# Performance work log

Measured on AMD Instinct MI355X. Metric: run time of the kernel, lower is better.

The kernel has to match this reference:

```python
import jax, jax.numpy as jnp
import numpy as np

B, T, C, H = 4, 2048, 1024, 16
D = C // H

def setup_inputs() -> dict:
    key = jax.random.key(0)
    k1, k2, k3, k4 = jax.random.split(key, 4)
    s = 1.0 / np.sqrt(C)
    return {
        "x": jax.random.normal(k1, (B, T, C), dtype=jnp.float32),
        "W_qkv": jax.random.normal(k2, (3 * C, C), dtype=jnp.float32) * s,
        "W_out": jax.random.normal(k3, (C, C), dtype=jnp.float32) * s,
        "b_out": jax.random.normal(k4, (C,), dtype=jnp.float32) * s,
    }

def reference(x, W_qkv, W_out, b_out):
    Bx, Tx, Cx = x.shape
    # qkv projection (torch Linear: y = x @ W.T), bias=False
    qkv = x @ W_qkv.T                               # [B,T,3C]
    q, k, v = jnp.split(qkv, 3, axis=-1)
    def heads(t):
        return t.reshape(Bx, Tx, H, D).transpose(0, 2, 1, 3)  # [B,H,T,D]
    q, k, v = heads(q), heads(k), heads(v)
    scale = 1.0 / jnp.sqrt(jnp.asarray(D, dtype=x.dtype))
    scores = jnp.einsum("bhqd,bhkd->bhqk", q, k) * scale      # [B,H,T,T]
    causal = jnp.tril(jnp.ones((Tx, Tx), dtype=bool))
    scores = jnp.where(causal[None, None], scores, -jnp.inf)
    attn = jax.nn.softmax(scores, axis=-1)                    # dropout p=0 (eval)
    out = jnp.einsum("bhqk,bhkd->bhqd", attn, v)              # [B,H,T,D]
    out = out.transpose(0, 2, 1, 3).reshape(Bx, Tx, Cx)       # [B,T,C]
    return out @ W_out.T + b_out
```

## Files before the change

kernel.cpp:

```cpp
#include <hip/hip_runtime.h>


typedef __attribute__((ext_vector_type(8))) __bf16 bf16x8;
typedef __attribute__((ext_vector_type(4))) float f32x4;
typedef __attribute__((ext_vector_type(16))) float f32x16;

__device__ __forceinline__ unsigned short f2bf(float f) {
  union { float f; unsigned u; } v; v.f = f;
  unsigned r = v.u + 0x7fffu + ((v.u >> 16) & 1u);
  return (unsigned short)(r >> 16);
}

__device__ __forceinline__ unsigned cvtpk(float lo, float hi) {
  unsigned r;
  asm("v_cvt_pk_bf16_f32 %0, %1, %2" : "=v"(r) : "v"(lo), "v"(hi));
  return r;
}

__device__ __forceinline__ float fexp2(float x) {
  float r;
  asm("v_exp_f32 %0, %1" : "=v"(r) : "v"(x));
  return r;
}
__device__ __forceinline__ float max3f(float a, float b, float c) {
  return fmaxf(fmaxf(a, b), c);
}

__device__ __forceinline__ void gld16(const void* g, void* l) {
  __builtin_amdgcn_global_load_lds(
      (const __attribute__((address_space(1))) void*)g,
      (__attribute__((address_space(3))) void*)l, 16, 0, 0);
}

__device__ __forceinline__ f32x4 mfma16(bf16x8 a, bf16x8 b, f32x4 c) {
  return __builtin_amdgcn_mfma_f32_16x16x32_bf16(a, b, c, 0, 0, 0);
}
__device__ __forceinline__ f32x16 mfma32(bf16x8 a, bf16x8 b, f32x16 c) {
  return __builtin_amdgcn_mfma_f32_32x32x16_bf16(a, b, c, 0, 0, 0);
}

__global__ __launch_bounds__(256) void cast_f32_bf16(
    const float* __restrict__ src, unsigned short* __restrict__ dst, int n) {
  int i = (blockIdx.x * 256 + threadIdx.x) * 4;
  if (i >= n) return;
  float4 v = *(const float4*)(src + i);
  ushort4 o;
  o.x = f2bf(v.x); o.y = f2bf(v.y); o.z = f2bf(v.z); o.w = f2bf(v.w);
  *(ushort4*)(dst + i) = o;
}

__device__ __forceinline__ bf16x8 ldsw128(const char* mat, int row, int cb) {
  return *(const bf16x8*)(mat + row * 128 + (cb ^ ((row & 7) << 4)));
}
__device__ __forceinline__ int swz512(int r) {
  return ((r & 7) << 4) ^ (((r >> 3) & 3) << 7);
}

#define PH_SYNC_A() do { __builtin_amdgcn_s_barrier();              \
    asm volatile("s_waitcnt lgkmcnt(0)" ::: "memory");              \
    __builtin_amdgcn_sched_barrier(0); } while (0)
#define PH_SYNC_B() do { __builtin_amdgcn_s_barrier();              \
    __builtin_amdgcn_sched_barrier(0); } while (0)
#define VMC6() asm volatile("s_waitcnt vmcnt(6)" ::: "memory")
#define VMC0() asm volatile("s_waitcnt vmcnt(0)" ::: "memory")

#define QUAD(MH, NH, AF, BF) do {                                   \
    __builtin_amdgcn_s_setprio(1);                                  \
    _Pragma("unroll") for (int mt = 0; mt < 4; ++mt)                \
    _Pragma("unroll") for (int nt = 0; nt < 2; ++nt)                \
    _Pragma("unroll") for (int kk = 0; kk < 2; ++kk)                \
      acc[(MH)*4+mt][(NH)*2+nt] =                                   \
          mfma16(AF[mt][kk], BF[nt][kk], acc[(MH)*4+mt][(NH)*2+nt]);\
    __builtin_amdgcn_s_setprio(0);                                  \
  } while (0)

__device__ __forceinline__ void stage_half(const char* gbase, char* mat,
                                           int kt, int half, int tid) {
#pragma unroll
  for (int q = 0; q < 2; ++q) {
    const int r = half * 128 + q * 64 + (tid >> 3);
    const int cb = (tid & 7) * 16;
    gld16(gbase + (size_t)r * 2048 + kt * 128 + (cb ^ ((r & 7) << 4)),
          mat + r * 128 + cb);
  }
}

__device__ __forceinline__ void rdA(bf16x8 aF[4][2], const char* mat,
                                    int wm, int mh, int lr, int lg) {
#pragma unroll
  for (int mt = 0; mt < 4; ++mt) {
    const int row = mh * 128 + wm * 64 + mt * 16 + lr;
#pragma unroll
    for (int kk = 0; kk < 2; ++kk)
      aF[mt][kk] = ldsw128(mat, row, kk * 64 + lg * 16);
  }
}
__device__ __forceinline__ void rdB(bf16x8 bF[2][2], const char* mat,
                                    int wn, int nh, int lr, int lg) {
#pragma unroll
  for (int nt = 0; nt < 2; ++nt) {
    const int row = wn * 64 + nh * 32 + nt * 16 + lr;
#pragma unroll
    for (int kk = 0; kk < 2; ++kk)
      bF[nt][kk] = ldsw128(mat, row, kk * 64 + lg * 16);
  }
}

template <int MODE>
__global__ __launch_bounds__(512, 2) void gemm8p(
    const unsigned short* __restrict__ A, const unsigned short* __restrict__ Bm,
    unsigned short* __restrict__ qo, unsigned short* __restrict__ ko,
    unsigned short* __restrict__ vo,
    const float* __restrict__ bias, float* __restrict__ fout) {
  __shared__ char lds[131072];
  const int tid = threadIdx.x;
  const int w = tid >> 6, l = tid & 63, lr = l & 15, lg = l >> 4;
  const int wm = w >> 2, wn = w & 3;
  constexpr int GX = (MODE == 0) ? 12 : 4;
  const int L = blockIdx.x + blockIdx.y * GX;
  const int x = L & 7, i8 = L >> 3;
  const int m0 = (x * 4 + (i8 & 3)) * 256;
  const int n0 = (i8 >> 2) * 256;
  const char* Ag = (const char*)A + (size_t)m0 * 2048;
  const char* Bg = (const char*)Bm + (size_t)n0 * 2048;
  char* A0 = lds;           char* B0 = lds + 32768;
  char* A1 = lds + 65536;   char* B1 = lds + 98304;

  f32x4 acc[8][4];
  f32x4 zero = {0.f, 0.f, 0.f, 0.f};
#pragma unroll
  for (int i = 0; i < 8; i++)
#pragma unroll
    for (int jj = 0; jj < 4; jj++) acc[i][jj] = zero;

  stage_half(Ag, A0, 0, 0, tid);
  stage_half(Ag, A0, 0, 1, tid);
  stage_half(Bg, B0, 0, 0, tid);
  stage_half(Bg, B0, 0, 1, tid);
  stage_half(Ag, A1, 1, 0, tid);
  stage_half(Bg, B1, 1, 0, tid);
  stage_half(Bg, B1, 1, 1, tid);
  VMC6();
  __builtin_amdgcn_s_barrier();
  __builtin_amdgcn_sched_barrier(0);

  for (int j = 0; j < 8; ++j) {
    const int t0 = 2 * j, t1 = 2 * j + 1;
    const bool more = (j < 7);
    bf16x8 aF[4][2], b0F[2][2], b1F[2][2];

    rdA(aF, A0, wm, 0, lr, lg);
    rdB(b0F, B0, wn, 0, lr, lg);
    stage_half(Ag, A1, t1, 1, tid);
    PH_SYNC_A();
    QUAD(0, 0, aF, b0F);
    PH_SYNC_B();
    rdB(b1F, B0, wn, 1, lr, lg);
    if (more) stage_half(Ag, A0, t0 + 2, 0, tid);
    PH_SYNC_A();
    QUAD(0, 1, aF, b1F);
    PH_SYNC_B();
    rdA(aF, A0, wm, 1, lr, lg);
    if (more) stage_half(Bg, B0, t0 + 2, 0, tid);
    PH_SYNC_A();
    QUAD(1, 1, aF, b1F);
    PH_SYNC_B();
    if (more) stage_half(Bg, B0, t0 + 2, 1, tid);
    PH_SYNC_A();
    QUAD(1, 0, aF, b0F);
    if (more) VMC6(); else VMC0();
    PH_SYNC_B();
    rdA(aF, A1, wm, 0, lr, lg);
    rdB(b0F, B1, wn, 0, lr, lg);
    if (more) stage_half(Ag, A0, t0 + 2, 1, tid);
    PH_SYNC_A();
    QUAD(0, 0, aF, b0F);
    PH_SYNC_B();
    rdB(b1F, B1, wn, 1, lr, lg);
    if (more) stage_half(Ag, A1, t1 + 2, 0, tid);
    PH_SYNC_A();
    QUAD(0, 1, aF, b1F);
    PH_SYNC_B();
    rdA(aF, A1, wm, 1, lr, lg);
    if (more) stage_half(Bg, B1, t1 + 2, 0, tid);
    PH_SYNC_A();
    QUAD(1, 1, aF, b1F);
    PH_SYNC_B();
    if (more) stage_half(Bg, B1, t1 + 2, 1, tid);
    PH_SYNC_A();
    QUAD(1, 0, aF, b0F);
    if (more) VMC6();
    PH_SYNC_B();
  }

  if (MODE == 1) {
#pragma unroll
    for (int mt8 = 0; mt8 < 8; ++mt8) {
      const int mh = mt8 >> 2, mt = mt8 & 3;
#pragma unroll
      for (int nt4 = 0; nt4 < 4; ++nt4) {
        int n = n0 + wn * 64 + nt4 * 16 + lr;
        int mbase = m0 + mh * 128 + wm * 64 + mt * 16 + lg * 4;
        float bv = bias[n];
#pragma unroll
        for (int i = 0; i < 4; i++)
          fout[(size_t)(mbase + i) * 1024 + n] = acc[mt8][nt4][i] + bv;
      }
    }
    return;
  }

  const int ty = n0 >> 10;
  const int hbase = (n0 & 1023) >> 6;
  const int bb = m0 >> 11;
  const int tloc = m0 & 2047;
  const float sc = (ty == 0) ? 0.18033688011111687f : 1.0f;

  if (ty < 2) {
#pragma unroll
    for (int mt8 = 0; mt8 < 8; ++mt8) {
      const int mh = mt8 >> 2, mt = mt8 & 3;
#pragma unroll
      for (int nt4 = 0; nt4 < 4; ++nt4) {
        const int col = wn * 64 + nt4 * 16 + lr;
#pragma unroll
        for (int i = 0; i < 4; ++i) {
          const int row = mh * 128 + wm * 64 + mt * 16 + lg * 4 + i;
          *(unsigned short*)(lds + row * 512 + ((col * 2) ^ swz512(row))) =
              f2bf(acc[mt8][nt4][i] * sc);
        }
      }
    }
    __builtin_amdgcn_s_barrier();
    unsigned short* dst = (ty == 0) ? qo : ko;
    const int hi = tid >> 7, r = tid & 127;
    unsigned short* gp =
        dst + (((size_t)(bb * 16 + hbase + hi)) * 2048 + tloc + 2 * r) * 64;
#pragma unroll
    for (int rr = 0; rr < 2; ++rr) {
      const int row = 2 * r + rr;
#pragma unroll
      for (int jc = 0; jc < 8; ++jc) {
        uint4 vd = *(const uint4*)(lds + row * 512 +
                                   ((hi * 128 + jc * 16) ^ swz512(row)));
        *(uint4*)(gp + rr * 64 + jc * 8) = vd;
      }
    }
  } else {
#pragma unroll
    for (int mt8 = 0; mt8 < 8; ++mt8) {
      const int mh = mt8 >> 2, mt = mt8 & 3;
      const int mcb = (mh * 128 + wm * 64 + mt * 16 + lg * 4) * 2;
#pragma unroll
      for (int nt4 = 0; nt4 < 4; ++nt4) {
        const int row = wn * 64 + nt4 * 16 + lr;
        uint2 pk;
        pk.x = cvtpk(acc[mt8][nt4][0], acc[mt8][nt4][1]);
        pk.y = cvtpk(acc[mt8][nt4][2], acc[mt8][nt4][3]);
        *(uint2*)(lds + row * 512 + (mcb ^ swz512(row))) = pk;
      }
    }
    __builtin_amdgcn_s_barrier();
    const int hi = tid >> 7, r = tid & 127;
    const int dd = r >> 1, mh2 = r & 1;
    const int nrow = hi * 64 + dd;
    unsigned short* gp = vo +
        (((size_t)(bb * 16 + hbase + hi)) * 64 + dd) * 2048 + tloc + mh2 * 128;
#pragma unroll
    for (int jc = 0; jc < 16; ++jc) {
      uint4 vd = *(const uint4*)(lds + nrow * 512 +
                                 ((mh2 * 256 + jc * 16) ^ swz512(nrow)));
      *(uint4*)(gp + jc * 8) = vd;
    }
  }
}

__device__ __forceinline__ bf16x8 ldsw(const char* base, int row, int cb) {
  return *(const bf16x8*)(base + row * 128 + (cb ^ ((row & 7) << 4)));
}

__global__ __launch_bounds__(512, 4) void attn_causal(
    const unsigned short* __restrict__ qg, const unsigned short* __restrict__ kg,
    const unsigned short* __restrict__ vtg, unsigned short* __restrict__ og) {
  __shared__ char lds[32768];
  const int tid = threadIdx.x;
  const int w = tid >> 6, l = tid & 63, lo = l & 31, hi = l >> 5;
  const int bh = blockIdx.x;
  const int qc = (0x31204657u >> (blockIdx.y * 4)) & 7;
  const int q0 = qc * 256;
  const int nkv = qc * 4 + 4;
  const int b = bh >> 4, h = bh & 15;
  const char* kpB = (const char*)(kg + (size_t)bh * 131072);
  const char* vpB = (const char*)(vtg + (size_t)bh * 131072);
  const unsigned short* qp = qg + (size_t)bh * 131072;
  const int qrow = q0 + 8 * lo + w;

  bf16x8 qf[4];
#pragma unroll
  for (int c = 0; c < 4; ++c)
    qf[c] = *(const bf16x8*)(qp + (size_t)qrow * 64 + hi * 8 + c * 16);

  f32x16 ov[2];
#pragma unroll
  for (int r = 0; r < 16; ++r) { ov[0][r] = 0.f; ov[1][r] = 0.f; }
  const f32x16 zz = {0.f, 0.f, 0.f, 0.f, 0.f, 0.f, 0.f, 0.f,
                     0.f, 0.f, 0.f, 0.f, 0.f, 0.f, 0.f, 0.f};
  float m = -__builtin_inff(), lsum = 0.f;

  const int srow = tid >> 3;
  const int scb = ((tid & 7) * 16) ^ ((srow & 7) << 4);

  gld16(kpB + (size_t)srow * 128 + scb, lds + tid * 16);
  gld16(vpB + (size_t)srow * 4096 + scb, lds + 8192 + tid * 16);
  __syncthreads();

  for (int kt = 0; kt < nkv; ++kt) {
    const int k0 = kt * 64;
    if (kt + 1 < nkv) {
      char* nb = lds + ((kt + 1) & 1) * 16384;
      gld16(kpB + (size_t)(k0 + 64 + srow) * 128 + scb, nb + tid * 16);
      gld16(vpB + (size_t)srow * 4096 + (size_t)(k0 + 64) * 2 + scb, nb + 8192 + tid * 16);
    }
    const char* Kbuf = lds + (kt & 1) * 16384;
    const char* Vbuf = Kbuf + 8192;

    f32x16 sv[2];
    __builtin_amdgcn_s_setprio(1);
#pragma unroll
    for (int c = 0; c < 4; ++c) {
      bf16x8 kf0 = ldsw(Kbuf, lo, hi * 16 + c * 32);
      bf16x8 kf1 = ldsw(Kbuf, 32 + lo, hi * 16 + c * 32);
      if (c == 0) {
        sv[0] = mfma32(kf0, qf[0], zz);
        sv[1] = mfma32(kf1, qf[0], zz);
      } else {
        sv[0] = mfma32(kf0, qf[c], sv[0]);
        sv[1] = mfma32(kf1, qf[c], sv[1]);
      }
    }
    __builtin_amdgcn_s_setprio(0);

    if (kt >= nkv - 4) {
#pragma unroll
      for (int t = 0; t < 2; ++t)
#pragma unroll
        for (int r = 0; r < 16; ++r) {
          int kgl = k0 + t * 32 + (r & 3) + 8 * (r >> 2) + 4 * hi;
          if (kgl > qrow) sv[t][r] = -__builtin_inff();
        }
    }

    float t0m = max3f(sv[0][0], sv[0][1], sv[0][2]);
    float t1m = max3f(sv[0][3], sv[0][4], sv[0][5]);
    float t2m = max3f(sv[0][6], sv[0][7], sv[0][8]);
    float t3m = max3f(sv[0][9], sv[0][10], sv[0][11]);
    float t4m = max3f(sv[0][12], sv[0][13], sv[0][14]);
    float t5m = max3f(sv[0][15], sv[1][0], sv[1][1]);
    float t6m = max3f(sv[1][2], sv[1][3], sv[1][4]);
    float t7m = max3f(sv[1][5], sv[1][6], sv[1][7]);
    float t8m = max3f(sv[1][8], sv[1][9], sv[1][10]);
    float t9m = max3f(sv[1][11], sv[1][12], sv[1][13]);
    float tam = fmaxf(sv[1][14], sv[1][15]);
    float u0 = max3f(t0m, t1m, t2m);
    float u1 = max3f(t3m, t4m, t5m);
    float u2 = max3f(t6m, t7m, t8m);
    float u3 = fmaxf(t9m, tam);
    float tm = fmaxf(max3f(u0, u1, u2), u3);
    tm = fmaxf(tm, __shfl_xor(tm, 32, 64));

    if (!__all(tm <= m + 8.f)) {
      float nm = fmaxf(fmaxf(m, tm), -1e30f);
      float f = fexp2(m - nm);
      m = nm;
      lsum *= f;
#pragma unroll
      for (int r = 0; r < 16; ++r) { ov[0][r] *= f; ov[1][r] *= f; }
    }

    float ps0 = 0.f, ps1 = 0.f, ps2 = 0.f, ps3 = 0.f;
#pragma unroll
    for (int t = 0; t < 2; ++t)
#pragma unroll
      for (int r = 0; r < 16; r += 4) {
        float p0 = fexp2(sv[t][r + 0] - m);
        float p1 = fexp2(sv[t][r + 1] - m);
        float p2 = fexp2(sv[t][r + 2] - m);
        float p3 = fexp2(sv[t][r + 3] - m);
        sv[t][r + 0] = p0; sv[t][r + 1] = p1;
        sv[t][r + 2] = p2; sv[t][r + 3] = p3;
        ps0 += p0; ps1 += p1; ps2 += p2; ps3 += p3;
      }
    lsum += (ps0 + ps1) + (ps2 + ps3);

    __builtin_amdgcn_s_setprio(1);
#pragma unroll
    for (int c = 0; c < 4; ++c) {
      const int t = c >> 1, rb = (c & 1) * 8;
      unsigned wA = cvtpk(sv[t][rb + 0], sv[t][rb + 1]);
      unsigned wB = cvtpk(sv[t][rb + 2], sv[t][rb + 3]);
      unsigned wC = cvtpk(sv[t][rb + 4], sv[t][rb + 5]);
      unsigned wD = cvtpk(sv[t][rb + 6], sv[t][rb + 7]);
      asm volatile("v_permlane32_swap_b32 %0, %1" : "+v"(wA), "+v"(wC));
      asm volatile("v_permlane32_swap_b32 %0, %1" : "+v"(wB), "+v"(wD));
      union { uint4 u; bf16x8 h; } pc;
      pc.u.x = wA; pc.u.y = wB; pc.u.z = wC; pc.u.w = wD;
      bf16x8 vf0 = ldsw(Vbuf, lo, hi * 16 + c * 32);
      bf16x8 vf1 = ldsw(Vbuf, 32 + lo, hi * 16 + c * 32);
      ov[0] = mfma32(vf0, pc.h, ov[0]);
      ov[1] = mfma32(vf1, pc.h, ov[1]);
    }
    __builtin_amdgcn_s_setprio(0);
    __syncthreads();
  }

  float lt = lsum + __shfl_xor(lsum, 32, 64);
  float inv = 1.0f / lt;
  char* outl = lds + w * 4096;
#pragma unroll
  for (int t2 = 0; t2 < 2; ++t2)
#pragma unroll
    for (int rp = 0; rp < 8; ++rp) {
      const int r = rp * 2;
      const int d0 = (r & 3) + 8 * (r >> 2) + 4 * hi + 32 * t2;
      unsigned pw = cvtpk(ov[t2][r] * inv, ov[t2][r + 1] * inv);
      *(unsigned*)(outl + lo * 128 + ((d0 * 2) ^ ((lo & 7) << 4))) = pw;
    }
  __syncthreads();
  {
    const int qi = l >> 1, cbb = (l & 1) * 64;
    const int t = q0 + 8 * qi + w;
    unsigned short* gp = og + ((size_t)(b * 2048 + t)) * 1024 + h * 64 + (cbb >> 1);
#pragma unroll
    for (int i = 0; i < 4; ++i) {
      uint4 vdat = *(const uint4*)(outl + qi * 128 + ((cbb + i * 16) ^ ((qi & 7) << 4)));
      *(uint4*)(gp + i * 8) = vdat;
    }
  }
}

extern "C" void kernel_launch(void* const* d_in, const int* in_sizes, int n_in,
                              void* d_out, int out_size, void* d_ws, size_t ws_size,
                              hipStream_t stream) {
  const float* x = (const float*)d_in[0];
  const float* Wqkv = (const float*)d_in[1];
  const float* Wout = (const float*)d_in[2];
  const float* bout = (const float*)d_in[3];
  float* out = (float*)d_out;
  char* ws = (char*)d_ws;

  unsigned short* xb = (unsigned short*)(ws);
  unsigned short* wqb = (unsigned short*)(ws + 16777216);
  unsigned short* wob = (unsigned short*)(ws + 23068672);
  unsigned short* qb = (unsigned short*)(ws + 25165824);
  unsigned short* kb = (unsigned short*)(ws + 41943040);
  unsigned short* vtb = (unsigned short*)(ws + 58720256);
  unsigned short* ogb = xb;

  cast_f32_bf16<<<8192, 256, 0, stream>>>(x, xb, 8388608);
  cast_f32_bf16<<<3072, 256, 0, stream>>>(Wqkv, wqb, 3145728);
  cast_f32_bf16<<<1024, 256, 0, stream>>>(Wout, wob, 1048576);

  gemm8p<0><<<dim3(12, 32), 512, 0, stream>>>(xb, wqb, qb, kb, vtb, nullptr, nullptr);
  attn_causal<<<dim3(64, 8), 512, 0, stream>>>(qb, kb, vtb, ogb);
  gemm8p<1><<<dim3(4, 32), 512, 0, stream>>>(ogb, wob, nullptr, nullptr, nullptr, bout, out);
}
```

Before: 172.0 us.

## Shrink GEMM tiles to 128x256 with simpler two-phase double-buffered pipeline

```diff
diff --git a/kernel.cpp b/kernel.cpp
--- a/kernel.cpp
+++ b/kernel.cpp
@@ -52,9 +52,6 @@
 __device__ __forceinline__ bf16x8 ldsw128(const char* mat, int row, int cb) {
   return *(const bf16x8*)(mat + row * 128 + (cb ^ ((row & 7) << 4)));
 }
-__device__ __forceinline__ int swz512(int r) {
-  return ((r & 7) << 4) ^ (((r >> 3) & 3) << 7);
-}
 
 #define PH_SYNC_A() do { __builtin_amdgcn_s_barrier();              \
     asm volatile("s_waitcnt lgkmcnt(0)" ::: "memory");              \
@@ -62,17 +59,8 @@
 #define PH_SYNC_B() do { __builtin_amdgcn_s_barrier();              \
     __builtin_amdgcn_sched_barrier(0); } while (0)
 #define VMC6() asm volatile("s_waitcnt vmcnt(6)" ::: "memory")
+#define VMC2() asm volatile("s_waitcnt vmcnt(2)" ::: "memory")
 #define VMC0() asm volatile("s_waitcnt vmcnt(0)" ::: "memory")
-
-#define QUAD(MH, NH, AF, BF) do {                                   \
-    __builtin_amdgcn_s_setprio(1);                                  \
-    _Pragma("unroll") for (int mt = 0; mt < 4; ++mt)                \
-    _Pragma("unroll") for (int nt = 0; nt < 2; ++nt)                \
-    _Pragma("unroll") for (int kk = 0; kk < 2; ++kk)                \
-      acc[(MH)*4+mt][(NH)*2+nt] =                                   \
-          mfma16(AF[mt][kk], BF[nt][kk], acc[(MH)*4+mt][(NH)*2+nt]);\
-    __builtin_amdgcn_s_setprio(0);                                  \
-  } while (0)
 
 __device__ __forceinline__ void stage_half(const char* gbase, char* mat,
                                            int kt, int half, int tid) {
@@ -84,127 +72,123 @@
           mat + r * 128 + cb);
   }
 }
-
-__device__ __forceinline__ void rdA(bf16x8 aF[4][2], const char* mat,
-                                    int wm, int mh, int lr, int lg) {
-#pragma unroll
-  for (int mt = 0; mt < 4; ++mt) {
-    const int row = mh * 128 + wm * 64 + mt * 16 + lr;
-#pragma unroll
-    for (int kk = 0; kk < 2; ++kk)
-      aF[mt][kk] = ldsw128(mat, row, kk * 64 + lg * 16);
-  }
-}
-__device__ __forceinline__ void rdB(bf16x8 bF[2][2], const char* mat,
-                                    int wn, int nh, int lr, int lg) {
-#pragma unroll
-  for (int nt = 0; nt < 2; ++nt) {
-    const int row = wn * 64 + nh * 32 + nt * 16 + lr;
-#pragma unroll
-    for (int kk = 0; kk < 2; ++kk)
-      bF[nt][kk] = ldsw128(mat, row, kk * 64 + lg * 16);
+__device__ __forceinline__ void stage_A(const char* gbase, char* mat,
+                                        int kt, int tid) {
+#pragma unroll
+  for (int q = 0; q < 2; ++q) {
+    const int r = q * 64 + (tid >> 3);
+    const int cb = (tid & 7) * 16;
+    gld16(gbase + (size_t)r * 2048 + kt * 128 + (cb ^ ((r & 7) << 4)),
+          mat + r * 128 + cb);
   }
 }
 
 template <int MODE>
-__global__ __launch_bounds__(512, 2) void gemm8p(
+__global__ __launch_bounds__(512, 2) void gemm2p(
     const unsigned short* __restrict__ A, const unsigned short* __restrict__ Bm,
     unsigned short* __restrict__ qo, unsigned short* __restrict__ ko,
     unsigned short* __restrict__ vo,
     const float* __restrict__ bias, float* __restrict__ fout) {
-  __shared__ char lds[131072];
+  __shared__ char lds[98304];
   const int tid = threadIdx.x;
   const int w = tid >> 6, l = tid & 63, lr = l & 15, lg = l >> 4;
   const int wm = w >> 2, wn = w & 3;
   constexpr int GX = (MODE == 0) ? 12 : 4;
+  constexpr int NWG = GX * 64;
   const int L = blockIdx.x + blockIdx.y * GX;
-  const int x = L & 7, i8 = L >> 3;
-  const int m0 = (x * 4 + (i8 & 3)) * 256;
-  const int n0 = (i8 >> 2) * 256;
+  const int logical = (L & 7) * (NWG >> 3) + (L >> 3);
+  const int m0 = (logical / GX) * 128, n0 = (logical % GX) * 256;
   const char* Ag = (const char*)A + (size_t)m0 * 2048;
   const char* Bg = (const char*)Bm + (size_t)n0 * 2048;
-  char* A0 = lds;           char* B0 = lds + 32768;
-  char* A1 = lds + 65536;   char* B1 = lds + 98304;
-
-  f32x4 acc[8][4];
+  char* A0 = lds;            char* A1 = lds + 16384;
+  char* B0 = lds + 32768;    char* B1 = lds + 65536;
+
+  f32x4 acc[4][4];
   f32x4 zero = {0.f, 0.f, 0.f, 0.f};
 #pragma unroll
-  for (int i = 0; i < 8; i++)
+  for (int i = 0; i < 4; i++)
 #pragma unroll
     for (int jj = 0; jj < 4; jj++) acc[i][jj] = zero;
 
-  stage_half(Ag, A0, 0, 0, tid);
-  stage_half(Ag, A0, 0, 1, tid);
+  stage_A(Ag, A0, 0, tid);
   stage_half(Bg, B0, 0, 0, tid);
   stage_half(Bg, B0, 0, 1, tid);
-  stage_half(Ag, A1, 1, 0, tid);
+  stage_A(Ag, A1, 1, tid);
   stage_half(Bg, B1, 1, 0, tid);
   stage_half(Bg, B1, 1, 1, tid);
   VMC6();
   __builtin_amdgcn_s_barrier();
   __builtin_amdgcn_sched_barrier(0);
 
-  for (int j = 0; j < 8; ++j) {
-    const int t0 = 2 * j, t1 = 2 * j + 1;
-    const bool more = (j < 7);
-    bf16x8 aF[4][2], b0F[2][2], b1F[2][2];
-
-    rdA(aF, A0, wm, 0, lr, lg);
-    rdB(b0F, B0, wn, 0, lr, lg);
-    stage_half(Ag, A1, t1, 1, tid);
+  for (int t = 0; t < 16; ++t) {
+    char* As = (t & 1) ? A1 : A0;
+    char* Bs = (t & 1) ? B1 : B0;
+    char* Bo = (t & 1) ? B0 : B1;
+    bf16x8 aF[4][2], bF[2][2];
+
+#pragma unroll
+    for (int mq = 0; mq < 4; ++mq) {
+      const int row = (mq >> 1) * 64 + wm * 32 + (mq & 1) * 16 + lr;
+#pragma unroll
+      for (int kk = 0; kk < 2; ++kk)
+        aF[mq][kk] = ldsw128(As, row, kk * 64 + lg * 16);
+    }
+#pragma unroll
+    for (int nt = 0; nt < 2; ++nt) {
+      const int row = wn * 64 + nt * 16 + lr;
+#pragma unroll
+      for (int kk = 0; kk < 2; ++kk)
+        bF[nt][kk] = ldsw128(Bs, row, kk * 64 + lg * 16);
+    }
+    if (t >= 1 && t < 15) {
+      stage_half(Bg, Bo, t + 1, 0, tid);
+      stage_half(Bg, Bo, t + 1, 1, tid);
+    }
     PH_SYNC_A();
-    QUAD(0, 0, aF, b0F);
+    __builtin_amdgcn_s_setprio(1);
+#pragma unroll
+    for (int mq = 0; mq < 4; ++mq)
+#pragma unroll
+      for (int nt = 0; nt < 2; ++nt)
+#pragma unroll
+        for (int kk = 0; kk < 2; ++kk)
+          acc[mq][nt] = mfma16(aF[mq][kk], bF[nt][kk], acc[mq][nt]);
+    __builtin_amdgcn_s_setprio(0);
     PH_SYNC_B();
-    rdB(b1F, B0, wn, 1, lr, lg);
-    if (more) stage_half(Ag, A0, t0 + 2, 0, tid);
+
+#pragma unroll
+    for (int nt = 0; nt < 2; ++nt) {
+      const int row = wn * 64 + (2 + nt) * 16 + lr;
+#pragma unroll
+      for (int kk = 0; kk < 2; ++kk)
+        bF[nt][kk] = ldsw128(Bs, row, kk * 64 + lg * 16);
+    }
+    if (t < 14) stage_A(Ag, As, t + 2, tid);
     PH_SYNC_A();
-    QUAD(0, 1, aF, b1F);
+    __builtin_amdgcn_s_setprio(1);
+#pragma unroll
+    for (int mq = 0; mq < 4; ++mq)
+#pragma unroll
+      for (int nt = 0; nt < 2; ++nt)
+#pragma unroll
+        for (int kk = 0; kk < 2; ++kk)
+          acc[mq][2 + nt] = mfma16(aF[mq][kk], bF[nt][kk], acc[mq][2 + nt]);
+    __builtin_amdgcn_s_setprio(0);
+    if (t < 14) VMC2(); else if (t < 15) VMC0();
     PH_SYNC_B();
-    rdA(aF, A0, wm, 1, lr, lg);
-    if (more) stage_half(Bg, B0, t0 + 2, 0, tid);
-    PH_SYNC_A();
-    QUAD(1, 1, aF, b1F);
-    PH_SYNC_B();
-    if (more) stage_half(Bg, B0, t0 + 2, 1, tid);
-    PH_SYNC_A();
-    QUAD(1, 0, aF, b0F);
-    if (more) VMC6(); else VMC0();
-    PH_SYNC_B();
-    rdA(aF, A1, wm, 0, lr, lg);
-    rdB(b0F, B1, wn, 0, lr, lg);
-    if (more) stage_half(Ag, A0, t0 + 2, 1, tid);
-    PH_SYNC_A();
-    QUAD(0, 0, aF, b0F);
-    PH_SYNC_B();
-    rdB(b1F, B1, wn, 1, lr, lg);
-    if (more) stage_half(Ag, A1, t1 + 2, 0, tid);
-    PH_SYNC_A();
-    QUAD(0, 1, aF, b1F);
-    PH_SYNC_B();
-    rdA(aF, A1, wm, 1, lr, lg);
-    if (more) stage_half(Bg, B1, t1 + 2, 0, tid);
-    PH_SYNC_A();
-    QUAD(1, 1, aF, b1F);
-    PH_SYNC_B();
-    if (more) stage_half(Bg, B1, t1 + 2, 1, tid);
-    PH_SYNC_A();
-    QUAD(1, 0, aF, b0F);
-    if (more) VMC6();
-    PH_SYNC_B();
   }
 
   if (MODE == 1) {
 #pragma unroll
-    for (int mt8 = 0; mt8 < 8; ++mt8) {
-      const int mh = mt8 >> 2, mt = mt8 & 3;
-#pragma unroll
-      for (int nt4 = 0; nt4 < 4; ++nt4) {
-        int n = n0 + wn * 64 + nt4 * 16 + lr;
-        int mbase = m0 + mh * 128 + wm * 64 + mt * 16 + lg * 4;
+    for (int mq = 0; mq < 4; ++mq) {
+#pragma unroll
+      for (int nt = 0; nt < 4; ++nt) {
+        int n = n0 + wn * 64 + nt * 16 + lr;
+        int mb = m0 + (mq >> 1) * 64 + wm * 32 + (mq & 1) * 16 + lg * 4;
         float bv = bias[n];
 #pragma unroll
         for (int i = 0; i < 4; i++)
-          fout[(size_t)(mbase + i) * 1024 + n] = acc[mt8][nt4][i] + bv;
+          fout[(size_t)(mb + i) * 1024 + n] = acc[mq][nt][i] + bv;
       }
     }
     return;
@@ -214,63 +198,47 @@
   const int hbase = (n0 & 1023) >> 6;
   const int bb = m0 >> 11;
   const int tloc = m0 & 2047;
-  const float sc = (ty == 0) ? 0.18033688011111687f : 1.0f;
 
   if (ty < 2) {
-#pragma unroll
-    for (int mt8 = 0; mt8 < 8; ++mt8) {
-      const int mh = mt8 >> 2, mt = mt8 & 3;
-#pragma unroll
-      for (int nt4 = 0; nt4 < 4; ++nt4) {
-        const int col = wn * 64 + nt4 * 16 + lr;
-#pragma unroll
-        for (int i = 0; i < 4; ++i) {
-          const int row = mh * 128 + wm * 64 + mt * 16 + lg * 4 + i;
-          *(unsigned short*)(lds + row * 512 + ((col * 2) ^ swz512(row))) =
-              f2bf(acc[mt8][nt4][i] * sc);
-        }
+    unsigned short* dst = (ty == 0) ? qo : ko;
+    const float sc = (ty == 0) ? 0.18033688011111687f : 1.0f;
+    const int h = hbase + wn;
+#pragma unroll
+    for (int mq = 0; mq < 4; ++mq) {
+#pragma unroll
+      for (int nt = 0; nt < 4; ++nt) {
+        const int dd = nt * 16 + lr;
+        const int trow = tloc + (mq >> 1) * 64 + wm * 32 + (mq & 1) * 16 + lg * 4;
+#pragma unroll
+        for (int i = 0; i < 4; i++)
+          dst[((size_t)(bb * 16 + h) * 2048 + trow + i) * 64 + dd] =
+              f2bf(acc[mq][nt][i] * sc);
       }
     }
-    __builtin_amdgcn_s_barrier();
-    unsigned short* dst = (ty == 0) ? qo : ko;
-    const int hi = tid >> 7, r = tid & 127;
-    unsigned short* gp =
-        dst + (((size_t)(bb * 16 + hbase + hi)) * 2048 + tloc + 2 * r) * 64;
-#pragma unroll
-    for (int rr = 0; rr < 2; ++rr) {
-      const int row = 2 * r + rr;
-#pragma unroll
-      for (int jc = 0; jc < 8; ++jc) {
-        uint4 vd = *(const uint4*)(lds + row * 512 +
-                                   ((hi * 128 + jc * 16) ^ swz512(row)));
-        *(uint4*)(gp + rr * 64 + jc * 8) = vd;
-      }
-    }
   } else {
 #pragma unroll
-    for (int mt8 = 0; mt8 < 8; ++mt8) {
-      const int mh = mt8 >> 2, mt = mt8 & 3;
-      const int mcb = (mh * 128 + wm * 64 + mt * 16 + lg * 4) * 2;
-#pragma unroll
-      for (int nt4 = 0; nt4 < 4; ++nt4) {
-        const int row = wn * 64 + nt4 * 16 + lr;
+    for (int mq = 0; mq < 4; ++mq) {
+      const int mcb = ((mq >> 1) * 64 + wm * 32 + (mq & 1) * 16 + lg * 4) * 2;
+#pragma unroll
+      for (int nt = 0; nt < 4; ++nt) {
+        const int row = wn * 64 + nt * 16 + lr;
         uint2 pk;
-        pk.x = cvtpk(acc[mt8][nt4][0], acc[mt8][nt4][1]);
-        pk.y = cvtpk(acc[mt8][nt4][2], acc[mt8][nt4][3]);
-        *(uint2*)(lds + row * 512 + (mcb ^ swz512(row))) = pk;
+        pk.x = cvtpk(acc[mq][nt][0], acc[mq][nt][1]);
+        pk.y = cvtpk(acc[mq][nt][2], acc[mq][nt][3]);
+        *(uint2*)(lds + row * 256 + (mcb ^ ((row & 15) << 4))) = pk;
       }
     }
     __builtin_amdgcn_s_barrier();
     const int hi = tid >> 7, r = tid & 127;
-    const int dd = r >> 1, mh2 = r & 1;
+    const int dd = r & 63, seg = r >> 6;
     const int nrow = hi * 64 + dd;
     unsigned short* gp = vo +
-        (((size_t)(bb * 16 + hbase + hi)) * 64 + dd) * 2048 + tloc + mh2 * 128;
-#pragma unroll
-    for (int jc = 0; jc < 16; ++jc) {
-      uint4 vd = *(const uint4*)(lds + nrow * 512 +
-                                 ((mh2 * 256 + jc * 16) ^ swz512(nrow)));
-      *(uint4*)(gp + jc * 8) = vd;
+        ((size_t)(bb * 16 + hbase + hi) * 64 + dd) * 2048 + tloc + seg * 64;
+#pragma unroll
+    for (int j = 0; j < 8; ++j) {
+      uint4 vd = *(const uint4*)(lds + nrow * 256 +
+                                 ((seg * 128 + j * 16) ^ ((nrow & 15) << 4)));
+      *(uint4*)(gp + j * 8) = vd;
     }
   }
 }
@@ -460,7 +428,7 @@
   cast_f32_bf16<<<3072, 256, 0, stream>>>(Wqkv, wqb, 3145728);
   cast_f32_bf16<<<1024, 256, 0, stream>>>(Wout, wob, 1048576);
 
-  gemm8p<0><<<dim3(12, 32), 512, 0, stream>>>(xb, wqb, qb, kb, vtb, nullptr, nullptr);
+  gemm2p<0><<<dim3(12, 64), 512, 0, stream>>>(xb, wqb, qb, kb, vtb, nullptr, nullptr);
   attn_causal<<<dim3(64, 8), 512, 0, stream>>>(qb, kb, vtb, ogb);
-  gemm8p<1><<<dim3(4, 32), 512, 0, stream>>>(ogb, wob, nullptr, nullptr, nullptr, bout, out);
-}
+  gemm2p<1><<<dim3(4, 64), 512, 0, stream>>>(ogb, wob, nullptr, nullptr, nullptr, bout, out);
+}
```

Measured after the change: 158.2 us. 8.0% less time.
